# Performance work log

Measured on AMD Instinct MI355X. Metric: run time of the kernel, lower is better.

The kernel has to match this reference:

```python
import jax, jax.numpy as jnp
import numpy as np

N_NODES = 100000
N_EDGES = 1600000
IN_CH = 128
OUT_CH = 128


def setup_inputs() -> dict:
    key = jax.random.key(0)
    k = jax.random.split(key, 6)
    x = jax.random.normal(k[0], (N_NODES, IN_CH), dtype=jnp.float32)
    edge_index = jax.random.randint(k[1], (2, N_EDGES), 0, N_NODES, dtype=jnp.int32)
    # GCNConv linear weights (glorot-ish scale) and biases
    W1 = jax.random.normal(k[2], (IN_CH, OUT_CH), dtype=jnp.float32) / np.sqrt(IN_CH)
    b1 = jnp.zeros((OUT_CH,), dtype=jnp.float32)
    W2 = jax.random.normal(k[3], (OUT_CH, OUT_CH), dtype=jnp.float32) / np.sqrt(OUT_CH)
    b2 = jnp.zeros((OUT_CH,), dtype=jnp.float32)
    return {"x": x, "edge_index": edge_index, "W1": W1, "b1": b1, "W2": W2, "b2": b2}


def gcn_conv(x, src, dst, W, b, n_nodes):
    """PyG GCNConv: add self-loops, symmetric D^-1/2 A D^-1/2 normalization."""
    h = x @ W  # [N, out]
    # degree including the implicit self-loop (weight 1)
    ones = jnp.ones(src.shape[0], dtype=x.dtype)
    deg = jax.ops.segment_sum(ones, dst, num_segments=n_nodes) + 1.0  # [N]
    dinv = jax.lax.rsqrt(deg)  # deg >= 1 so always finite
    coef = dinv[src] * dinv[dst]  # [E] edge norm 1/sqrt(d_i d_j)
    msg = h[src] * coef[:, None]  # [E, out] gather + scale
    agg = jax.ops.segment_sum(msg, dst, num_segments=n_nodes)  # scatter-add
    # self-loop contribution: norm = dinv[i]^2
    agg = agg + h * (dinv * dinv)[:, None]
    return agg + b


def reference(x, edge_index, W1, b1, W2, b2):
    src, dst = edge_index[0], edge_index[1]
    h = jax.nn.relu(gcn_conv(x, src, dst, W1, b1, N_NODES))
    out = jax.nn.relu(gcn_conv(h, src, dst, W2, b2, N_NODES))
    return out
```

## Files before the change

### kernel.cpp

```cpp
#include <hip/hip_runtime.h>


#define NN 100000
#define NBKT 512
#define BKT_W 196
#define CHUNK 8192
#define CAP 6144

__device__ __forceinline__ ushort f2bf(float f) {
  unsigned u = __float_as_uint(f);
  unsigned r = (u + 0x7fffu + ((u >> 16) & 1u)) >> 16;
  return (ushort)r;
}
__device__ __forceinline__ float bf2f(ushort s) {
  return __uint_as_float(((unsigned)s) << 16);
}


__global__ __launch_bounds__(512) void kb_hist(const int* __restrict__ dst,
                                               int* __restrict__ bcnt, int E) {
  __shared__ int h[NBKT];
  for (int i = threadIdx.x; i < NBKT; i += 512) h[i] = 0;
  __syncthreads();
  int base = blockIdx.x * CHUNK;
#pragma unroll 4
  for (int q = 0; q < CHUNK / 512; q++) {
    int e = base + threadIdx.x + q * 512;
    if (e < E) atomicAdd(&h[dst[e] / BKT_W], 1);
  }
  __syncthreads();
  for (int i = threadIdx.x; i < NBKT; i += 512)
    if (h[i]) atomicAdd(&bcnt[i], h[i]);
}

__global__ __launch_bounds__(512) void kb_scan(const int* __restrict__ bcnt,
                                               int* __restrict__ bbase,
                                               int* __restrict__ bcur,
                                               int* __restrict__ row_ptr,
                                               int N, int E) {
  __shared__ int s[NBKT];
  int t = threadIdx.x;
  int v = bcnt[t];
  s[t] = v;
  __syncthreads();
  for (int off = 1; off < NBKT; off <<= 1) {
    int x = (t >= off) ? s[t - off] : 0;
    __syncthreads();
    s[t] += x;
    __syncthreads();
  }
  int ex = s[t] - v;
  bbase[t] = ex;
  bcur[t] = ex;
  if (t == NBKT - 1) bbase[NBKT] = E;
  if (t == 0) row_ptr[N] = E;
}

__global__ __launch_bounds__(512) void kb_scatter(const int* __restrict__ src,
                                                  const int* __restrict__ dst,
                                                  int* __restrict__ bcur,
                                                  int2* __restrict__ pairs, int E) {
  __shared__ int h[NBKT];
  __shared__ int gb[NBKT];
  for (int i = threadIdx.x; i < NBKT; i += 512) h[i] = 0;
  __syncthreads();

  const int base = blockIdx.x * CHUNK;
  const int t = threadIdx.x;
  int rank[CHUNK / 512], bkt[CHUNK / 512], sv[CHUNK / 512], dv[CHUNK / 512];
#pragma unroll
  for (int q = 0; q < CHUNK / 512; q++) {
    int e = base + t + q * 512;
    if (e < E) {
      int d = dst[e];
      int b = d / BKT_W;
      bkt[q] = b;
      sv[q] = src[e];
      dv[q] = d;
      rank[q] = atomicAdd(&h[b], 1);
    } else {
      bkt[q] = -1;
    }
  }
  __syncthreads();
  for (int i = t; i < NBKT; i += 512) {
    int c = h[i];
    gb[i] = c ? atomicAdd(&bcur[i], c) : 0;
  }
  __syncthreads();
#pragma unroll
  for (int q = 0; q < CHUNK / 512; q++) {
    if (bkt[q] >= 0) pairs[(size_t)gb[bkt[q]] + rank[q]] = make_int2(sv[q], dv[q]);
  }
}

__global__ __launch_bounds__(512) void kb_sort(const int* __restrict__ bbase,
                                               const int2* __restrict__ pairs,
                                               int* __restrict__ csr_src,
                                               int* __restrict__ row_ptr,
                                               int N, int E) {
  __shared__ int cnt[256];
  __shared__ int sc[256];
  __shared__ int cur[256];
  __shared__ int stage[CAP];

  const int b = blockIdx.x;
  const int t = threadIdx.x;
  const int lo = bbase[b], hi = bbase[b + 1];
  const int n0 = b * BKT_W;
  int m = hi - lo;
  if (m > CAP) m = CAP;

  if (t < 256) cnt[t] = 0;
  __syncthreads();

  for (int i = t; i < m; i += 512) {
    int2 p = pairs[(size_t)lo + i];
    atomicAdd(&cnt[p.y - n0], 1);
  }
  __syncthreads();

  int v = 0;
  if (t < 256) {
    v = cnt[t];
    sc[t] = v;
  }
  __syncthreads();
  for (int off = 1; off < 256; off <<= 1) {
    int x = 0;
    if (t < 256 && t >= off) x = sc[t - off];
    __syncthreads();
    if (t < 256) sc[t] += x;
    __syncthreads();
  }
  if (t < 256) {
    int ex = sc[t] - v;
    cur[t] = ex;
    int node = n0 + t;
    if (t < BKT_W && node < N) row_ptr[node] = lo + ex;
  }
  __syncthreads();

  for (int i = t; i < m; i += 512) {
    int2 p = pairs[(size_t)lo + i];
    int pos = atomicAdd(&cur[p.y - n0], 1);
    stage[pos] = p.x;
  }
  __syncthreads();

  for (int i = t; i < m; i += 512) csr_src[(size_t)lo + i] = stage[i];
}

__global__ __launch_bounds__(256) void k_dinv(const int* __restrict__ row_ptr,
                                              float* __restrict__ dinv, int N) {
  int i = blockIdx.x * 256 + threadIdx.x;
  if (i < N) dinv[i] = rsqrtf((float)(row_ptr[i + 1] - row_ptr[i]) + 1.0f);
}

#define KC 32
__global__ __launch_bounds__(256) void k_gemm128(const float* __restrict__ X,
                                                 const float* __restrict__ W,
                                                 const float* __restrict__ dinv,
                                                 ushort* __restrict__ hs, int M) {
  __shared__ float xs[KC][68];
  __shared__ float wt[KC][132];

  const int t = threadIdx.x;
  const int row0 = blockIdx.x * 64;
  const int trow = t >> 4;
  const int tcol = t & 15;

  float acc[4][8];
#pragma unroll
  for (int i = 0; i < 4; i++)
#pragma unroll
    for (int j = 0; j < 8; j++) acc[i][j] = 0.f;

  for (int k0 = 0; k0 < 128; k0 += KC) {
    {
      int r = t >> 2;
      int kk = (t & 3) * 8;
      int grow = row0 + r;
      float4 v0, v1;
      if (grow < M) {
        const float* p = X + (size_t)grow * 128 + k0 + kk;
        v0 = *(const float4*)p;
        v1 = *(const float4*)(p + 4);
      } else {
        v0 = make_float4(0.f, 0.f, 0.f, 0.f);
        v1 = v0;
      }
      xs[kk + 0][r] = v0.x; xs[kk + 1][r] = v0.y;
      xs[kk + 2][r] = v0.z; xs[kk + 3][r] = v0.w;
      xs[kk + 4][r] = v1.x; xs[kk + 5][r] = v1.y;
      xs[kk + 6][r] = v1.z; xs[kk + 7][r] = v1.w;
    }
    {
#pragma unroll
      for (int q = 0; q < 4; q++) {
        int f4 = t + q * 256;
        int k = f4 >> 5;
        int c4 = f4 & 31;
        float4 v = *(const float4*)(W + (size_t)(k0 + k) * 128 + c4 * 4);
        *(float4*)&wt[k][c4 * 4] = v;
      }
    }
    __syncthreads();

#pragma unroll
    for (int k = 0; k < KC; k++) {
      float4 a = *(const float4*)&xs[k][trow * 4];
      float4 w0 = *(const float4*)&wt[k][tcol * 8];
      float4 w1 = *(const float4*)&wt[k][tcol * 8 + 4];
      float av[4] = {a.x, a.y, a.z, a.w};
      float wv[8] = {w0.x, w0.y, w0.z, w0.w, w1.x, w1.y, w1.z, w1.w};
#pragma unroll
      for (int i = 0; i < 4; i++)
#pragma unroll
        for (int j = 0; j < 8; j++) acc[i][j] = fmaf(av[i], wv[j], acc[i][j]);
    }
    __syncthreads();
  }

#pragma unroll
  for (int i = 0; i < 4; i++) {
    int r = row0 + trow * 4 + i;
    if (r < M) {
      float sc = dinv[r];
      ushort u[8];
#pragma unroll
      for (int j = 0; j < 8; j++) u[j] = f2bf(acc[i][j] * sc);
      *(uint4*)(hs + (size_t)r * 128 + tcol * 8) = *(uint4*)u;
    }
  }
}

__global__ __launch_bounds__(256) void k_agg(const int* __restrict__ row_ptr,
                                             const int* __restrict__ csr_src,
                                             const float* __restrict__ dinv,
                                             const ushort* __restrict__ hs,
                                             const float* __restrict__ bias,
                                             float* __restrict__ out, int N) {
  const int node = blockIdx.x * 4 + (threadIdx.x >> 6);
  if (node >= N) return;
  const int lane = threadIdx.x & 63;
  const ushort2* hp = (const ushort2*)hs;

  const int e0 = row_ptr[node];
  const int e1 = row_ptr[node + 1];

  float ax = 0.f, ay = 0.f;
  int e = e0;
  for (; e + 4 <= e1; e += 4) {
    int s0 = csr_src[e];
    int s1 = csr_src[e + 1];
    int s2 = csr_src[e + 2];
    int s3 = csr_src[e + 3];
    ushort2 v0 = hp[(size_t)s0 * 64 + lane];
    ushort2 v1 = hp[(size_t)s1 * 64 + lane];
    ushort2 v2 = hp[(size_t)s2 * 64 + lane];
    ushort2 v3 = hp[(size_t)s3 * 64 + lane];
    ax += bf2f(v0.x) + bf2f(v1.x) + bf2f(v2.x) + bf2f(v3.x);
    ay += bf2f(v0.y) + bf2f(v1.y) + bf2f(v2.y) + bf2f(v3.y);
  }
  for (; e < e1; ++e) {
    int s = csr_src[e];
    ushort2 v = hp[(size_t)s * 64 + lane];
    ax += bf2f(v.x);
    ay += bf2f(v.y);
  }
  {
    ushort2 v = hp[(size_t)node * 64 + lane];
    ax += bf2f(v.x);
    ay += bf2f(v.y);
  }
  float dv = dinv[node];
  float2 bv = ((const float2*)bias)[lane];
  float2 o;
  o.x = fmaxf(fmaf(ax, dv, bv.x), 0.f);
  o.y = fmaxf(fmaf(ay, dv, bv.y), 0.f);
  ((float2*)out)[(size_t)node * 64 + lane] = o;
}


extern "C" void kernel_launch(void* const* d_in, const int* in_sizes, int n_in,
                              void* d_out, int out_size, void* d_ws, size_t ws_size,
                              hipStream_t stream) {
  const float* x  = (const float*)d_in[0];
  const int*   ei = (const int*)d_in[1];
  const float* W1 = (const float*)d_in[2];
  const float* b1 = (const float*)d_in[3];
  const float* W2 = (const float*)d_in[4];
  const float* b2 = (const float*)d_in[5];
  float* out = (float*)d_out;

  const int N = NN;
  const int E = in_sizes[1] / 2;
  const int* src = ei;
  const int* dst = ei + E;

  char* w = (char*)d_ws;
  auto alloc = [&](size_t bytes) {
    char* p = w;
    w += (bytes + 255) & ~(size_t)255;
    return p;
  };
  float*  dinv    = (float*)alloc((size_t)N * 4);
  int*    row_ptr = (int*)alloc((size_t)(N + 1) * 4);
  int*    bcnt    = (int*)alloc(NBKT * 4);
  int*    bbase   = (int*)alloc((NBKT + 1) * 4);
  int*    bcur    = (int*)alloc(NBKT * 4);
  int*    csr_src = (int*)alloc((size_t)E * 4);
  int2*   pairs   = (int2*)alloc((size_t)E * 8);
  ushort* hs      = (ushort*)alloc((size_t)N * 128 * 2);

  const int EB = (E + CHUNK - 1) / CHUNK;

  hipMemsetAsync(bcnt, 0, NBKT * 4, stream);
  kb_hist<<<EB, 512, 0, stream>>>(dst, bcnt, E);
  kb_scan<<<1, 512, 0, stream>>>(bcnt, bbase, bcur, row_ptr, N, E);
  kb_scatter<<<EB, 512, 0, stream>>>(src, dst, bcur, pairs, E);
  kb_sort<<<NBKT, 512, 0, stream>>>(bbase, pairs, csr_src, row_ptr, N, E);
  k_dinv<<<(N + 255) / 256, 256, 0, stream>>>(row_ptr, dinv, N);

  const int NAGG = (N + 3) / 4;

  k_gemm128<<<(N + 63) / 64, 256, 0, stream>>>(x, W1, dinv, hs, N);
  k_agg<<<NAGG, 256, 0, stream>>>(row_ptr, csr_src, dinv, hs, b1, out, N);
  k_gemm128<<<(N + 63) / 64, 256, 0, stream>>>(out, W2, dinv, hs, N);
  k_agg<<<NAGG, 256, 0, stream>>>(row_ptr, csr_src, dinv, hs, b2, out, N);
}
```

Baseline: 383.7 us.

## Replace FP32 FMA GEMM with split-bf16 MFMA GEMM and unroll aggregation gather

The scalar FP32 tiled GEMM is replaced by a matrix-core kernel. It splits X and W into bf16 hi/lo parts and accumulates three MFMA products to keep near-fp32 accuracy. W is converted once per block into swizzled LDS, and X fragments are read straight from global memory. The aggregation loop is also unrolled from 4 to 8 gathers to put more loads in flight. The output store is now per-element ushort writes, which are less coalesced, and each block pays the 64KB W conversion up front.

```diff
diff --git a/kernel.cpp b/kernel.cpp
--- a/kernel.cpp
+++ b/kernel.cpp
@@ -7,6 +7,9 @@
 #define CHUNK 8192
 #define CAP 6144
 
+typedef __attribute__((ext_vector_type(8))) short bf16x8;
+typedef __attribute__((ext_vector_type(4))) float f32x4;
+
 __device__ __forceinline__ ushort f2bf(float f) {
   unsigned u = __float_as_uint(f);
   unsigned r = (u + 0x7fffu + ((u >> 16) & 1u)) >> 16;
@@ -14,6 +17,9 @@
 }
 __device__ __forceinline__ float bf2f(ushort s) {
   return __uint_as_float(((unsigned)s) << 16);
+}
+__device__ __forceinline__ unsigned hipair(unsigned ue, unsigned uo) {
+  return (uo & 0xffff0000u) | (ue >> 16);
 }
 
 
@@ -157,80 +163,113 @@
   if (i < N) dinv[i] = rsqrtf((float)(row_ptr[i + 1] - row_ptr[i]) + 1.0f);
 }
 
-#define KC 32
-__global__ __launch_bounds__(256) void k_gemm128(const float* __restrict__ X,
-                                                 const float* __restrict__ W,
-                                                 const float* __restrict__ dinv,
-                                                 ushort* __restrict__ hs, int M) {
-  __shared__ float xs[KC][68];
-  __shared__ float wt[KC][132];
+
+__device__ __forceinline__ void cvt_row(const float* __restrict__ p,
+                                        bf16x8* hi, bf16x8* lo) {
+  float4 v0 = *(const float4*)p;
+  float4 v1 = *(const float4*)(p + 4);
+  float f[8] = {v0.x, v0.y, v0.z, v0.w, v1.x, v1.y, v1.z, v1.w};
+  unsigned hw[4], lw[4];
+#pragma unroll
+  for (int i = 0; i < 4; ++i) {
+    unsigned u0 = __float_as_uint(f[2 * i]);
+    unsigned u1 = __float_as_uint(f[2 * i + 1]);
+    float l0 = f[2 * i] - __uint_as_float(u0 & 0xffff0000u);
+    float l1 = f[2 * i + 1] - __uint_as_float(u1 & 0xffff0000u);
+    hw[i] = hipair(u0, u1);
+    lw[i] = hipair(__float_as_uint(l0), __float_as_uint(l1));
+  }
+  uint4 H = make_uint4(hw[0], hw[1], hw[2], hw[3]);
+  uint4 L = make_uint4(lw[0], lw[1], lw[2], lw[3]);
+  *hi = __builtin_bit_cast(bf16x8, H);
+  *lo = __builtin_bit_cast(bf16x8, L);
+}
+
+__global__ __launch_bounds__(256) void k_gemm_mfma(const float* __restrict__ X,
+                                                   const float* __restrict__ W,
+                                                   const float* __restrict__ dinv,
+                                                   ushort* __restrict__ hs, int M) {
+  __shared__ ushort wt_hi[128 * 128];
+  __shared__ ushort wt_lo[128 * 128];
 
   const int t = threadIdx.x;
-  const int row0 = blockIdx.x * 64;
-  const int trow = t >> 4;
-  const int tcol = t & 15;
-
-  float acc[4][8];
-#pragma unroll
-  for (int i = 0; i < 4; i++)
-#pragma unroll
-    for (int j = 0; j < 8; j++) acc[i][j] = 0.f;
-
-  for (int k0 = 0; k0 < 128; k0 += KC) {
-    {
-      int r = t >> 2;
-      int kk = (t & 3) * 8;
-      int grow = row0 + r;
-      float4 v0, v1;
-      if (grow < M) {
-        const float* p = X + (size_t)grow * 128 + k0 + kk;
-        v0 = *(const float4*)p;
-        v1 = *(const float4*)(p + 4);
-      } else {
-        v0 = make_float4(0.f, 0.f, 0.f, 0.f);
-        v1 = v0;
+
+  {
+    const int n4 = (t & 31) * 4;
+    const int kq0 = (t >> 5) * 4;
+    for (int it = 0; it < 4; ++it) {
+      const int kq = kq0 + it * 32;
+      float4 r[4];
+#pragma unroll
+      for (int j = 0; j < 4; ++j)
+        r[j] = *(const float4*)(W + (size_t)(kq + j) * 128 + n4);
+#pragma unroll
+      for (int q = 0; q < 4; ++q) {
+        const int n = n4 + q;
+        unsigned u[4], l[4];
+#pragma unroll
+        for (int j = 0; j < 4; ++j) {
+          float f = ((const float*)&r[j])[q];
+          u[j] = __float_as_uint(f);
+          float lf = f - __uint_as_float(u[j] & 0xffff0000u);
+          l[j] = __float_as_uint(lf);
+        }
+        uint2 hw = make_uint2(hipair(u[0], u[1]), hipair(u[2], u[3]));
+        uint2 lw = make_uint2(hipair(l[0], l[1]), hipair(l[2], l[3]));
+        const int bo = (n * 256 + kq * 2) ^ ((n & 7) << 4);
+        *(uint2*)((char*)wt_hi + bo) = hw;
+        *(uint2*)((char*)wt_lo + bo) = lw;
       }
-      xs[kk + 0][r] = v0.x; xs[kk + 1][r] = v0.y;
-      xs[kk + 2][r] = v0.z; xs[kk + 3][r] = v0.w;
-      xs[kk + 4][r] = v1.x; xs[kk + 5][r] = v1.y;
-      xs[kk + 6][r] = v1.z; xs[kk + 7][r] = v1.w;
-    }
-    {
-#pragma unroll
-      for (int q = 0; q < 4; q++) {
-        int f4 = t + q * 256;
-        int k = f4 >> 5;
-        int c4 = f4 & 31;
-        float4 v = *(const float4*)(W + (size_t)(k0 + k) * 128 + c4 * 4);
-        *(float4*)&wt[k][c4 * 4] = v;
+    }
+  }
+  __syncthreads();
+
+  const int wv = t >> 6;
+  const int lane = t & 63;
+  const int r0 = blockIdx.x * 128 + wv * 32;
+  const int la = lane & 15;
+  const int kg = (lane >> 4) * 8;
+  const int rowA = min(r0 + la, M - 1);
+  const int rowB = min(r0 + 16 + la, M - 1);
+
+  f32x4 acc[2][8];
+#pragma unroll
+  for (int rs = 0; rs < 2; ++rs)
+#pragma unroll
+    for (int ct = 0; ct < 8; ++ct) acc[rs][ct] = (f32x4)(0.f);
+
+#pragma unroll
+  for (int ks = 0; ks < 4; ++ks) {
+    const int koff = ks * 32 + kg;
+    bf16x8 ah0, al0, ah1, al1;
+    cvt_row(X + (size_t)rowA * 128 + koff, &ah0, &al0);
+    cvt_row(X + (size_t)rowB * 128 + koff, &ah1, &al1);
+#pragma unroll
+    for (int ct = 0; ct < 8; ++ct) {
+      const int n = ct * 16 + la;
+      const int bo = (n * 256 + koff * 2) ^ ((n & 7) << 4);
+      bf16x8 bh = *(const bf16x8*)((const char*)wt_hi + bo);
+      bf16x8 bl = *(const bf16x8*)((const char*)wt_lo + bo);
+      acc[0][ct] = __builtin_amdgcn_mfma_f32_16x16x32_bf16(ah0, bh, acc[0][ct], 0, 0, 0);
+      acc[0][ct] = __builtin_amdgcn_mfma_f32_16x16x32_bf16(ah0, bl, acc[0][ct], 0, 0, 0);
+      acc[0][ct] = __builtin_amdgcn_mfma_f32_16x16x32_bf16(al0, bh, acc[0][ct], 0, 0, 0);
+      acc[1][ct] = __builtin_amdgcn_mfma_f32_16x16x32_bf16(ah1, bh, acc[1][ct], 0, 0, 0);
+      acc[1][ct] = __builtin_amdgcn_mfma_f32_16x16x32_bf16(ah1, bl, acc[1][ct], 0, 0, 0);
+      acc[1][ct] = __builtin_amdgcn_mfma_f32_16x16x32_bf16(al1, bh, acc[1][ct], 0, 0, 0);
+    }
+  }
+
+#pragma unroll
+  for (int rs = 0; rs < 2; ++rs) {
+#pragma unroll
+    for (int j = 0; j < 4; ++j) {
+      int r = r0 + rs * 16 + (lane >> 4) * 4 + j;
+      if (r < M) {
+        float sc = dinv[r];
+#pragma unroll
+        for (int ct = 0; ct < 8; ++ct)
+          hs[(size_t)r * 128 + ct * 16 + la] = f2bf(acc[rs][ct][j] * sc);
       }
-    }
-    __syncthreads();
-
-#pragma unroll
-    for (int k = 0; k < KC; k++) {
-      float4 a = *(const float4*)&xs[k][trow * 4];
-      float4 w0 = *(const float4*)&wt[k][tcol * 8];
-      float4 w1 = *(const float4*)&wt[k][tcol * 8 + 4];
-      float av[4] = {a.x, a.y, a.z, a.w};
-      float wv[8] = {w0.x, w0.y, w0.z, w0.w, w1.x, w1.y, w1.z, w1.w};
-#pragma unroll
-      for (int i = 0; i < 4; i++)
-#pragma unroll
-        for (int j = 0; j < 8; j++) acc[i][j] = fmaf(av[i], wv[j], acc[i][j]);
-    }
-    __syncthreads();
-  }
-
-#pragma unroll
-  for (int i = 0; i < 4; i++) {
-    int r = row0 + trow * 4 + i;
-    if (r < M) {
-      float sc = dinv[r];
-      ushort u[8];
-#pragma unroll
-      for (int j = 0; j < 8; j++) u[j] = f2bf(acc[i][j] * sc);
-      *(uint4*)(hs + (size_t)r * 128 + tcol * 8) = *(uint4*)u;
     }
   }
 }
@@ -251,17 +290,18 @@
 
   float ax = 0.f, ay = 0.f;
   int e = e0;
-  for (; e + 4 <= e1; e += 4) {
-    int s0 = csr_src[e];
-    int s1 = csr_src[e + 1];
-    int s2 = csr_src[e + 2];
-    int s3 = csr_src[e + 3];
-    ushort2 v0 = hp[(size_t)s0 * 64 + lane];
-    ushort2 v1 = hp[(size_t)s1 * 64 + lane];
-    ushort2 v2 = hp[(size_t)s2 * 64 + lane];
-    ushort2 v3 = hp[(size_t)s3 * 64 + lane];
-    ax += bf2f(v0.x) + bf2f(v1.x) + bf2f(v2.x) + bf2f(v3.x);
-    ay += bf2f(v0.y) + bf2f(v1.y) + bf2f(v2.y) + bf2f(v3.y);
+  for (; e + 8 <= e1; e += 8) {
+    int s[8];
+#pragma unroll
+    for (int q = 0; q < 8; q++) s[q] = csr_src[e + q];
+    ushort2 v[8];
+#pragma unroll
+    for (int q = 0; q < 8; q++) v[q] = hp[(size_t)s[q] * 64 + lane];
+#pragma unroll
+    for (int q = 0; q < 8; q++) {
+      ax += bf2f(v[q].x);
+      ay += bf2f(v[q].y);
+    }
   }
   for (; e < e1; ++e) {
     int s = csr_src[e];
@@ -324,9 +364,10 @@
   k_dinv<<<(N + 255) / 256, 256, 0, stream>>>(row_ptr, dinv, N);
 
   const int NAGG = (N + 3) / 4;
-
-  k_gemm128<<<(N + 63) / 64, 256, 0, stream>>>(x, W1, dinv, hs, N);
+  const int GB = (N + 127) / 128;
+
+  k_gemm_mfma<<<GB, 256, 0, stream>>>(x, W1, dinv, hs, N);
   k_agg<<<NAGG, 256, 0, stream>>>(row_ptr, csr_src, dinv, hs, b1, out, N);
-  k_gemm128<<<(N + 63) / 64, 256, 0, stream>>>(out, W2, dinv, hs, N);
+  k_gemm_mfma<<<GB, 256, 0, stream>>>(out, W2, dinv, hs, N);
   k_agg<<<NAGG, 256, 0, stream>>>(row_ptr, csr_src, dinv, hs, b2, out, N);
 }
```

Result: faster. 345.1 us (-10.1%).
